# Kernel optimization log

Hardware: AMD Instinct MI355X
Metric: run time of the kernel (lower is better)

The kernel has to match this reference:

```python
import jax, jax.numpy as jnp
import numpy as np

C, S, H = 64, 2048, 512
ITERATIONS = 3

def squash(x, eps=1e-07):
    # per-vector squash along last dim: (|x|^2/(1+|x|^2)) * x/|x|
    sq = jnp.sum(x * x, axis=-1, keepdims=True)
    safe_norm = jnp.sqrt(sq + eps)
    scale = sq / (1.0 + sq)
    return scale * (x / safe_norm)

def setup_inputs() -> dict:
    key = jax.random.key(0)
    k1, k2 = jax.random.split(key)
    x = jax.random.normal(k1, (C * S, H), dtype=jnp.float32)
    # xavier-normal init for Linear(H, H)
    std = np.sqrt(2.0 / (H + H)).astype(np.float32)
    W_weight = jax.random.normal(k2, (H, H), dtype=jnp.float32) * std
    W_bias = jnp.zeros((H,), dtype=jnp.float32)
    return {"x": x, "W_weight": W_weight, "W_bias": W_bias}

def reference(x, W_weight, W_bias):
    xr = x.reshape(C, S, H)
    # e_ij = squash(Linear(x))  -> [C, S, H]
    e_ij = squash(jnp.einsum('csh,oh->cso', xr, W_weight) + W_bias)
    b_ij = jnp.zeros((C, S), dtype=x.dtype)
    c_i = jnp.zeros((C, H), dtype=x.dtype)
    for _ in range(ITERATIONS):
        d_i = jax.nn.softmax(b_ij, axis=1)[..., None]          # [C, S, 1]
        c_i = squash(jnp.sum(d_i * e_ij, axis=1))              # [C, H]
        b_ij = b_ij + jnp.einsum('csh,ch->cs', e_ij, c_i)      # [C, S]
    return c_i
```

## Files before the change

### kernel.cpp

```cpp
#include <hip/hip_runtime.h>
#include <hip/hip_fp16.h>

#define HDIM 512

typedef __fp16 fp16x2 __attribute__((ext_vector_type(2)));
typedef _Float16 h8 __attribute__((ext_vector_type(8)));
typedef __attribute__((ext_vector_type(4))) float floatx4;

__device__ __forceinline__ void lds_barrier() {
  asm volatile("s_waitcnt lgkmcnt(0)\n\ts_barrier" ::: "memory");
}
__device__ __forceinline__ void issue_fence() {
  asm volatile("" ::: "memory");
}

__global__ __launch_bounds__(256) void prep_w_kernel(
    const float* __restrict__ W, _Float16* __restrict__ wf) {
  int i = (blockIdx.x * 256 + threadIdx.x) * 4;
  float4 f = *(const float4*)(W + i);
  wf[i + 0] = (_Float16)f.x;
  wf[i + 1] = (_Float16)f.y;
  wf[i + 2] = (_Float16)f.z;
  wf[i + 3] = (_Float16)f.w;
}

__device__ __forceinline__ void issue_w_dma(const _Float16* wf, _Float16* dst,
                                            int col0, int kt, int widx,
                                            int wn_sub, int wphys) {
#pragma unroll
  for (int q = 0; q < 4; ++q) {
    int i = widx * 4 + q;
    int n_loc = 8 * i + wn_sub;
    int kg_l = wphys ^ (n_loc & 7);
    size_t goff = (size_t)(col0 + n_loc) * HDIM + kt * 64 + kg_l * 8;
    __builtin_amdgcn_global_load_lds(
        (const __attribute__((address_space(1))) void*)(wf + goff),
        (__attribute__((address_space(3))) void*)(dst + i * 512), 16, 0, 0);
  }
}

__global__ __launch_bounds__(256) void gemm_kernel(
    const float* __restrict__ x, const _Float16* __restrict__ wf,
    const float* __restrict__ bias, __half* __restrict__ y,
    float* __restrict__ sq) {
  __shared__ _Float16 xs[128 * 64];
  __shared__ _Float16 wsm[2][128 * 64];

  const int tid = threadIdx.x;
  const int lane = tid & 63;
  const int widx = tid >> 6;
  const int wave_m = widx >> 1, wave_n = widx & 1;
  const int lrow = lane & 15, quad = lane >> 4, l7 = lane & 7;

  const int bid = blockIdx.x;
  const int m_blk = ((bid >> 5) << 3) + (bid & 7);
  const int n_blk = (bid >> 3) & 3;
  const int row0 = m_blk * 128;
  const int col0 = n_blk * 128;
  const int kt0 = bid & 7;

  floatx4 acc[4][4];
#pragma unroll
  for (int i = 0; i < 4; ++i)
#pragma unroll
    for (int j = 0; j < 4; ++j) acc[i][j] = (floatx4){0.f, 0.f, 0.f, 0.f};

  const int xm = tid >> 3;
  const int xkg = tid & 7;
  const int wn_sub = lane >> 3;
  const int wphys = lane & 7;

  const float* xbase = x + (size_t)row0 * HDIM + xkg * 8;
  float4 xr[2][4][2];

  issue_w_dma(wf, &wsm[0][0], col0, kt0, widx, wn_sub, wphys);
  issue_fence();
#pragma unroll
  for (int p = 0; p < 4; ++p) {
    const float* gp = xbase + (size_t)(p * 32 + xm) * HDIM + kt0 * 64;
    xr[0][p][0] = *(const float4*)gp;
    xr[0][p][1] = *(const float4*)(gp + 4);
  }
  issue_fence();
#pragma unroll
  for (int p = 0; p < 4; ++p) {
    const float* gp =
        xbase + (size_t)(p * 32 + xm) * HDIM + ((kt0 + 1) & 7) * 64;
    xr[1][p][0] = *(const float4*)gp;
    xr[1][p][1] = *(const float4*)(gp + 4);
  }

#pragma unroll
  for (int i = 0; i < 8; ++i) {
    lds_barrier();
#pragma unroll
    for (int p = 0; p < 4; ++p) {
      int m = p * 32 + xm;
      union { h8 v8; fp16x2 v2[4]; } u;
      u.v2[0] = __builtin_amdgcn_cvt_pkrtz(xr[i & 1][p][0].x, xr[i & 1][p][0].y);
      u.v2[1] = __builtin_amdgcn_cvt_pkrtz(xr[i & 1][p][0].z, xr[i & 1][p][0].w);
      u.v2[2] = __builtin_amdgcn_cvt_pkrtz(xr[i & 1][p][1].x, xr[i & 1][p][1].y);
      u.v2[3] = __builtin_amdgcn_cvt_pkrtz(xr[i & 1][p][1].z, xr[i & 1][p][1].w);
      int phys = xkg ^ (m & 7);
      *(h8*)&xs[m * 64 + phys * 8] = u.v8;
    }
    lds_barrier();
    if (i < 7)
      issue_w_dma(wf, &wsm[(i + 1) & 1][0], col0, (kt0 + i + 1) & 7, widx,
                  wn_sub, wphys);
    issue_fence();
    if (i < 6) {
      const int ktn = (kt0 + i + 2) & 7;
#pragma unroll
      for (int p = 0; p < 4; ++p) {
        const float* gp = xbase + (size_t)(p * 32 + xm) * HDIM + ktn * 64;
        xr[i & 1][p][0] = *(const float4*)gp;
        xr[i & 1][p][1] = *(const float4*)(gp + 4);
      }
    }
    if (i >= 1 && i <= 5) asm volatile("s_waitcnt vmcnt(20)" ::: "memory");
    if (i == 6) asm volatile("s_waitcnt vmcnt(12)" ::: "memory");
    if (i == 7) asm volatile("s_waitcnt vmcnt(0)" ::: "memory");
    const _Float16* wcur = &wsm[i & 1][0];
#pragma unroll
    for (int ks = 0; ks < 2; ++ks) {
      int physA = (ks * 4 + quad) ^ l7;
      h8 a[4], bh[4];
#pragma unroll
      for (int mt = 0; mt < 4; ++mt) {
        int r = wave_m * 64 + mt * 16 + lrow;
        a[mt] = *(const h8*)&xs[r * 64 + physA * 8];
      }
#pragma unroll
      for (int nt = 0; nt < 4; ++nt) {
        int c = wave_n * 64 + nt * 16 + lrow;
        bh[nt] = *(const h8*)&wcur[c * 64 + physA * 8];
      }
#pragma unroll
      for (int mt = 0; mt < 4; ++mt)
#pragma unroll
        for (int nt = 0; nt < 4; ++nt)
          acc[mt][nt] = __builtin_amdgcn_mfma_f32_16x16x32_f16(
              a[mt], bh[nt], acc[mt][nt], 0, 0, 0);
    }
  }

  int colg[4];
  float bias_v[4];
#pragma unroll
  for (int nt = 0; nt < 4; ++nt) {
    colg[nt] = col0 + wave_n * 64 + nt * 16 + lrow;
    bias_v[nt] = bias[colg[nt]];
  }
#pragma unroll
  for (int mt = 0; mt < 4; ++mt) {
#pragma unroll
    for (int r = 0; r < 4; ++r) {
      int rowg = row0 + wave_m * 64 + mt * 16 + quad * 4 + r;
      float s = 0.f;
#pragma unroll
      for (int nt = 0; nt < 4; ++nt) {
        float yv = acc[mt][nt][r] + bias_v[nt];
        s += yv * yv;
        y[(size_t)rowg * HDIM + colg[nt]] = __float2half(yv);
      }
      s += __shfl_xor(s, 1, 64);
      s += __shfl_xor(s, 2, 64);
      s += __shfl_xor(s, 4, 64);
      s += __shfl_xor(s, 8, 64);
      if (lrow == 0) atomicAdd(&sq[rowg], s);
    }
  }
}

__global__ __launch_bounds__(256) void kbv_kernel(
    const __half* __restrict__ y, const float* __restrict__ sqbuf,
    float* __restrict__ b, const float* __restrict__ c_buf,
    float* __restrict__ u_part, float* __restrict__ den_part) {
  const int w = threadIdx.x >> 6;
  const int lane = threadIdx.x & 63;
  const int wave_g = blockIdx.x * 4 + w;
  const int cap = wave_g >> 6;
  const int chunk = wave_g & 63;
  const int r0 = cap * 2048 + chunk * 32;

  float c8[8];
  {
    const float4* cp = (const float4*)(c_buf + cap * HDIM + lane * 8);
    float4 ca = cp[0], cb = cp[1];
    c8[0] = ca.x; c8[1] = ca.y; c8[2] = ca.z; c8[3] = ca.w;
    c8[4] = cb.x; c8[5] = cb.y; c8[6] = cb.z; c8[7] = cb.w;
  }
  float u8[8] = {0, 0, 0, 0, 0, 0, 0, 0};
  float den = 0.f;

  union U { int4 v; __half hh[8]; };
  U cur[4], nxt[4];
  const __half* yb = y + (size_t)r0 * HDIM + lane * 8;
#pragma unroll
  for (int j = 0; j < 4; ++j) cur[j].v = *(const int4*)(yb + (size_t)j * HDIM);

  for (int g = 0; g < 8; ++g) {
    const int rg = r0 + g * 4;
    if (g < 7) {
#pragma unroll
      for (int j = 0; j < 4; ++j)
        nxt[j].v = *(const int4*)(yb + (size_t)(g * 4 + 4 + j) * HDIM);
    }
    float sc[4], bv[4];
#pragma unroll
    for (int j = 0; j < 4; ++j) {
      float s = sqbuf[rg + j];
      sc[j] = s / ((1.f + s) * sqrtf(s + 1e-7f));
      bv[j] = b[rg + j];
    }
    float dot[4];
#pragma unroll
    for (int j = 0; j < 4; ++j) {
      float d = 0.f;
#pragma unroll
      for (int k = 0; k < 8; ++k) d += __half2float(cur[j].hh[k]) * c8[k];
      dot[j] = d;
    }
#pragma unroll
    for (int s = 1; s < 64; s <<= 1) {
#pragma unroll
      for (int j = 0; j < 4; ++j) dot[j] += __shfl_xor(dot[j], s, 64);
    }
#pragma unroll
    for (int j = 0; j < 4; ++j) {
      float bn = bv[j] + sc[j] * dot[j];
      if (lane == 0) b[rg + j] = bn;
      float wj = __expf(bn);
      den += wj;
      float wsc = wj * sc[j];
#pragma unroll
      for (int k = 0; k < 8; ++k) u8[k] += wsc * __half2float(cur[j].hh[k]);
    }
#pragma unroll
    for (int j = 0; j < 4; ++j) cur[j] = nxt[j];
  }

  __shared__ float lred[4][512];
  __shared__ float ldn[4];
#pragma unroll
  for (int k = 0; k < 8; ++k) lred[w][lane * 8 + k] = u8[k];
  if (lane == 0) ldn[w] = den;
  __syncthreads();
  const int t = threadIdx.x;
  const int blkc = blockIdx.x & 15;
#pragma unroll
  for (int hh = 0; hh < 2; ++hh) {
    int h = hh * 256 + t;
    float v = lred[0][h] + lred[1][h] + lred[2][h] + lred[3][h];
    u_part[((size_t)cap * 16 + blkc) * HDIM + h] = v;
  }
  if (t == 0)
    den_part[cap * 16 + blkc] = ldn[0] + ldn[1] + ldn[2] + ldn[3];
}

__global__ __launch_bounds__(512) void kcsq_kernel(
    const float* __restrict__ u_part, const float* __restrict__ den_part,
    float* __restrict__ out) {
  const int cap = blockIdx.x;
  const int t = threadIdx.x;
  __shared__ float red[512];
  __shared__ float sden;

  if (t < 16) red[t] = den_part[cap * 16 + t];
  __syncthreads();
  if (t == 0) {
    float s = 0.f;
#pragma unroll
    for (int i = 0; i < 16; ++i) s += red[i];
    sden = s;
  }
  __syncthreads();
  const float den = sden;

  float v = 0.f;
  const float* up = u_part + (size_t)cap * 16 * HDIM + t;
#pragma unroll
  for (int ch = 0; ch < 16; ++ch) v += up[ch * HDIM];
  v /= den;

  red[t] = v * v;
  __syncthreads();
  for (int s = 256; s > 0; s >>= 1) {
    if (t < s) red[t] += red[t + s];
    __syncthreads();
  }
  const float sqv = red[0];
  const float scv = sqv / ((1.f + sqv) * sqrtf(sqv + 1e-7f));
  out[cap * HDIM + t] = v * scv;
}

extern "C" void kernel_launch(void* const* d_in, const int* in_sizes, int n_in,
                              void* d_out, int out_size, void* d_ws,
                              size_t ws_size, hipStream_t stream) {
  const float* x = (const float*)d_in[0];
  const float* W = (const float*)d_in[1];
  const float* bias = (const float*)d_in[2];
  float* out = (float*)d_out;
  char* ws = (char*)d_ws;

  __half* y = (__half*)ws;
  float* sq = (float*)(ws + (size_t)134217728);
  float* b = sq + 131072;
  float* c_buf = b + 131072;
  _Float16* wf = (_Float16*)(c_buf + 32768);
  float* u_part = (float*)(wf + 262144);
  float* den_part = u_part + (size_t)64 * 16 * 512;

  (void)hipMemsetAsync(sq, 0,
                       (size_t)(131072 + 131072 + 32768) * sizeof(float),
                       stream);

  prep_w_kernel<<<256, 256, 0, stream>>>(W, wf);
  gemm_kernel<<<4096, 256, 0, stream>>>(x, wf, bias, y, sq);

  for (int it = 0; it < 3; ++it) {
    kbv_kernel<<<1024, 256, 0, stream>>>(y, sq, b, c_buf, u_part, den_part);
    kcsq_kernel<<<64, 512, 0, stream>>>(u_part, den_part,
                                        (it == 2) ? out : c_buf);
  }
}
```

Baseline: 535.4 us.

## Fuse squash and first routing iteration into full-width GEMM epilogue

```diff
diff --git a/kernel.cpp b/kernel.cpp
--- a/kernel.cpp
+++ b/kernel.cpp
@@ -24,159 +24,177 @@
   wf[i + 3] = (_Float16)f.w;
 }
 
-__device__ __forceinline__ void issue_w_dma(const _Float16* wf, _Float16* dst,
-                                            int col0, int kt, int widx,
-                                            int wn_sub, int wphys) {
+#define XS_H (128 * 40)
+#define WS_H (512 * 32)
+
+__device__ __forceinline__ void issue_w_dma(const _Float16* __restrict__ wf,
+                                            _Float16* dst, int kt, int tid,
+                                            int widx) {
 #pragma unroll
   for (int q = 0; q < 4; ++q) {
-    int i = widx * 4 + q;
-    int n_loc = 8 * i + wn_sub;
-    int kg_l = wphys ^ (n_loc & 7);
-    size_t goff = (size_t)(col0 + n_loc) * HDIM + kt * 64 + kg_l * 8;
+    int idx = q * 512 + tid;
+    int n = idx >> 2;
+    int src = (idx & 3) ^ ((n >> 1) & 3);
+    size_t goff = (size_t)n * HDIM + kt * 32 + src * 8;
     __builtin_amdgcn_global_load_lds(
         (const __attribute__((address_space(1))) void*)(wf + goff),
-        (__attribute__((address_space(3))) void*)(dst + i * 512), 16, 0, 0);
-  }
-}
-
-__global__ __launch_bounds__(256) void gemm_kernel(
+        (__attribute__((address_space(3))) void*)(dst +
+                                                  (q * 512 + widx * 64) * 8),
+        16, 0, 0);
+  }
+}
+
+__global__ __launch_bounds__(512, 2) void gemm_kernel(
     const float* __restrict__ x, const _Float16* __restrict__ wf,
-    const float* __restrict__ bias, __half* __restrict__ y,
-    float* __restrict__ sq) {
-  __shared__ _Float16 xs[128 * 64];
-  __shared__ _Float16 wsm[2][128 * 64];
+    const float* __restrict__ bias, __half* __restrict__ e,
+    float* __restrict__ u_part, float* __restrict__ den_part) {
+  __shared__ __align__(16) _Float16 smem[2 * XS_H + 3 * WS_H];
+  _Float16* xs[2] = {smem, smem + XS_H};
+  _Float16* wsm = smem + 2 * XS_H;
 
   const int tid = threadIdx.x;
   const int lane = tid & 63;
   const int widx = tid >> 6;
-  const int wave_m = widx >> 1, wave_n = widx & 1;
-  const int lrow = lane & 15, quad = lane >> 4, l7 = lane & 7;
+  const int wave_m = widx >> 2;
+  const int wave_n = widx & 3;
+  const int lrow = lane & 15, quad = lane >> 4;
 
   const int bid = blockIdx.x;
-  const int m_blk = ((bid >> 5) << 3) + (bid & 7);
-  const int n_blk = (bid >> 3) & 3;
-  const int row0 = m_blk * 128;
-  const int col0 = n_blk * 128;
-  const int kt0 = bid & 7;
-
-  floatx4 acc[4][4];
+  const int row0 = bid * 128;
+
+  const int xrow = tid >> 2;
+  const int xcg = tid & 3;
+  const float* xbase = x + (size_t)(row0 + xrow) * HDIM + xcg * 8;
+
+  floatx4 acc[4][8];
 #pragma unroll
   for (int i = 0; i < 4; ++i)
 #pragma unroll
-    for (int j = 0; j < 4; ++j) acc[i][j] = (floatx4){0.f, 0.f, 0.f, 0.f};
-
-  const int xm = tid >> 3;
-  const int xkg = tid & 7;
-  const int wn_sub = lane >> 3;
-  const int wphys = lane & 7;
-
-  const float* xbase = x + (size_t)row0 * HDIM + xkg * 8;
-  float4 xr[2][4][2];
-
-  issue_w_dma(wf, &wsm[0][0], col0, kt0, widx, wn_sub, wphys);
+    for (int j = 0; j < 8; ++j) acc[i][j] = (floatx4){0.f, 0.f, 0.f, 0.f};
+
+  float4 xr[2][2];
+
+  issue_w_dma(wf, wsm + 0 * WS_H, 0, tid, widx);
   issue_fence();
-#pragma unroll
-  for (int p = 0; p < 4; ++p) {
-    const float* gp = xbase + (size_t)(p * 32 + xm) * HDIM + kt0 * 64;
-    xr[0][p][0] = *(const float4*)gp;
-    xr[0][p][1] = *(const float4*)(gp + 4);
-  }
+  xr[0][0] = *(const float4*)xbase;
+  xr[0][1] = *(const float4*)(xbase + 4);
   issue_fence();
-#pragma unroll
-  for (int p = 0; p < 4; ++p) {
-    const float* gp =
-        xbase + (size_t)(p * 32 + xm) * HDIM + ((kt0 + 1) & 7) * 64;
-    xr[1][p][0] = *(const float4*)gp;
-    xr[1][p][1] = *(const float4*)(gp + 4);
-  }
-
-#pragma unroll
-  for (int i = 0; i < 8; ++i) {
+  issue_w_dma(wf, wsm + 1 * WS_H, 1, tid, widx);
+  issue_fence();
+  xr[1][0] = *(const float4*)(xbase + 32);
+  xr[1][1] = *(const float4*)(xbase + 36);
+  issue_fence();
+
+  const int chunkB = quad ^ ((lrow >> 1) & 3);
+
+#pragma unroll
+  for (int t = 0; t < 16; ++t) {
+    {
+      float4 a0 = xr[t & 1][0], a1 = xr[t & 1][1];
+      union { h8 v8; fp16x2 v2[4]; } u;
+      u.v2[0] = __builtin_amdgcn_cvt_pkrtz(a0.x, a0.y);
+      u.v2[1] = __builtin_amdgcn_cvt_pkrtz(a0.z, a0.w);
+      u.v2[2] = __builtin_amdgcn_cvt_pkrtz(a1.x, a1.y);
+      u.v2[3] = __builtin_amdgcn_cvt_pkrtz(a1.z, a1.w);
+      *(h8*)&xs[t & 1][xrow * 40 + xcg * 8] = u.v8;
+    }
     lds_barrier();
-#pragma unroll
-    for (int p = 0; p < 4; ++p) {
-      int m = p * 32 + xm;
-      union { h8 v8; fp16x2 v2[4]; } u;
-      u.v2[0] = __builtin_amdgcn_cvt_pkrtz(xr[i & 1][p][0].x, xr[i & 1][p][0].y);
-      u.v2[1] = __builtin_amdgcn_cvt_pkrtz(xr[i & 1][p][0].z, xr[i & 1][p][0].w);
-      u.v2[2] = __builtin_amdgcn_cvt_pkrtz(xr[i & 1][p][1].x, xr[i & 1][p][1].y);
-      u.v2[3] = __builtin_amdgcn_cvt_pkrtz(xr[i & 1][p][1].z, xr[i & 1][p][1].w);
-      int phys = xkg ^ (m & 7);
-      *(h8*)&xs[m * 64 + phys * 8] = u.v8;
-    }
-    lds_barrier();
-    if (i < 7)
-      issue_w_dma(wf, &wsm[(i + 1) & 1][0], col0, (kt0 + i + 1) & 7, widx,
-                  wn_sub, wphys);
-    issue_fence();
-    if (i < 6) {
-      const int ktn = (kt0 + i + 2) & 7;
-#pragma unroll
-      for (int p = 0; p < 4; ++p) {
-        const float* gp = xbase + (size_t)(p * 32 + xm) * HDIM + ktn * 64;
-        xr[i & 1][p][0] = *(const float4*)gp;
-        xr[i & 1][p][1] = *(const float4*)(gp + 4);
-      }
-    }
-    if (i >= 1 && i <= 5) asm volatile("s_waitcnt vmcnt(20)" ::: "memory");
-    if (i == 6) asm volatile("s_waitcnt vmcnt(12)" ::: "memory");
-    if (i == 7) asm volatile("s_waitcnt vmcnt(0)" ::: "memory");
-    const _Float16* wcur = &wsm[i & 1][0];
-#pragma unroll
-    for (int ks = 0; ks < 2; ++ks) {
-      int physA = (ks * 4 + quad) ^ l7;
-      h8 a[4], bh[4];
-#pragma unroll
-      for (int mt = 0; mt < 4; ++mt) {
-        int r = wave_m * 64 + mt * 16 + lrow;
-        a[mt] = *(const h8*)&xs[r * 64 + physA * 8];
-      }
-#pragma unroll
-      for (int nt = 0; nt < 4; ++nt) {
-        int c = wave_n * 64 + nt * 16 + lrow;
-        bh[nt] = *(const h8*)&wcur[c * 64 + physA * 8];
-      }
-#pragma unroll
-      for (int mt = 0; mt < 4; ++mt)
-#pragma unroll
-        for (int nt = 0; nt < 4; ++nt)
-          acc[mt][nt] = __builtin_amdgcn_mfma_f32_16x16x32_f16(
-              a[mt], bh[nt], acc[mt][nt], 0, 0, 0);
-    }
-  }
-
-  int colg[4];
-  float bias_v[4];
-#pragma unroll
-  for (int nt = 0; nt < 4; ++nt) {
-    colg[nt] = col0 + wave_n * 64 + nt * 16 + lrow;
+    if (t <= 13) {
+      issue_w_dma(wf, wsm + ((t + 2) % 3) * WS_H, t + 2, tid, widx);
+      issue_fence();
+      const float* gp = xbase + (t + 2) * 32;
+      xr[t & 1][0] = *(const float4*)gp;
+      xr[t & 1][1] = *(const float4*)(gp + 4);
+      issue_fence();
+    }
+    const _Float16* xsr = xs[t & 1];
+    const _Float16* wcur = wsm + (t % 3) * WS_H;
+    h8 a[4], bh[8];
+#pragma unroll
+    for (int mt = 0; mt < 4; ++mt)
+      a[mt] = *(const h8*)&xsr[(wave_m * 64 + mt * 16 + lrow) * 40 + quad * 8];
+#pragma unroll
+    for (int nt = 0; nt < 8; ++nt)
+      bh[nt] =
+          *(const h8*)&wcur[(wave_n * 128 + nt * 16 + lrow) * 32 + chunkB * 8];
+    __builtin_amdgcn_s_setprio(1);
+#pragma unroll
+    for (int mt = 0; mt < 4; ++mt)
+#pragma unroll
+      for (int nt = 0; nt < 8; ++nt)
+        acc[mt][nt] = __builtin_amdgcn_mfma_f32_16x16x32_f16(
+            a[mt], bh[nt], acc[mt][nt], 0, 0, 0);
+    __builtin_amdgcn_s_setprio(0);
+  }
+
+  float* sqp = (float*)smem;
+  float* scs = (float*)smem + 512;
+  float* upl = (float*)smem + 640;
+
+  float bias_v[8];
+  int colg[8];
+#pragma unroll
+  for (int nt = 0; nt < 8; ++nt) {
+    colg[nt] = wave_n * 128 + nt * 16 + lrow;
     bias_v[nt] = bias[colg[nt]];
   }
 #pragma unroll
   for (int mt = 0; mt < 4; ++mt) {
 #pragma unroll
     for (int r = 0; r < 4; ++r) {
-      int rowg = row0 + wave_m * 64 + mt * 16 + quad * 4 + r;
       float s = 0.f;
 #pragma unroll
-      for (int nt = 0; nt < 4; ++nt) {
+      for (int nt = 0; nt < 8; ++nt) {
         float yv = acc[mt][nt][r] + bias_v[nt];
         s += yv * yv;
-        y[(size_t)rowg * HDIM + colg[nt]] = __float2half(yv);
       }
       s += __shfl_xor(s, 1, 64);
       s += __shfl_xor(s, 2, 64);
       s += __shfl_xor(s, 4, 64);
       s += __shfl_xor(s, 8, 64);
-      if (lrow == 0) atomicAdd(&sq[rowg], s);
-    }
-  }
+      if (lrow == 0)
+        sqp[wave_n * 128 + wave_m * 64 + mt * 16 + quad * 4 + r] = s;
+    }
+  }
+  lds_barrier();
+  if (tid < 128) {
+    float s = sqp[tid] + sqp[128 + tid] + sqp[256 + tid] + sqp[384 + tid];
+    scs[tid] = s / ((1.f + s) * sqrtf(s + 1e-7f));
+  }
+  lds_barrier();
+
+  float up[8] = {0.f, 0.f, 0.f, 0.f, 0.f, 0.f, 0.f, 0.f};
+#pragma unroll
+  for (int mt = 0; mt < 4; ++mt) {
+#pragma unroll
+    for (int r = 0; r < 4; ++r) {
+      int row_local = wave_m * 64 + mt * 16 + quad * 4 + r;
+      float scv = scs[row_local];
+      __half* erow = e + (size_t)(row0 + row_local) * HDIM;
+#pragma unroll
+      for (int nt = 0; nt < 8; ++nt) {
+        float ev = (acc[mt][nt][r] + bias_v[nt]) * scv;
+        erow[colg[nt]] = __float2half(ev);
+        up[nt] += ev;
+      }
+    }
+  }
+#pragma unroll
+  for (int nt = 0; nt < 8; ++nt) {
+    float v = up[nt];
+    v += __shfl_xor(v, 16, 64);
+    v += __shfl_xor(v, 32, 64);
+    if (quad == 0) upl[wave_m * 512 + colg[nt]] = v;
+  }
+  lds_barrier();
+  u_part[(size_t)bid * HDIM + tid] = upl[tid] + upl[512 + tid];
+  if (tid == 0) den_part[bid] = 128.0f;
 }
 
 __global__ __launch_bounds__(256) void kbv_kernel(
-    const __half* __restrict__ y, const float* __restrict__ sqbuf,
-    float* __restrict__ b, const float* __restrict__ c_buf,
-    float* __restrict__ u_part, float* __restrict__ den_part) {
+    const __half* __restrict__ e, float* __restrict__ b,
+    const float* __restrict__ c_buf, float* __restrict__ u_part,
+    float* __restrict__ den_part) {
   const int w = threadIdx.x >> 6;
   const int lane = threadIdx.x & 63;
   const int wave_g = blockIdx.x * 4 + w;
@@ -196,7 +214,7 @@
 
   union U { int4 v; __half hh[8]; };
   U cur[4], nxt[4];
-  const __half* yb = y + (size_t)r0 * HDIM + lane * 8;
+  const __half* yb = e + (size_t)r0 * HDIM + lane * 8;
 #pragma unroll
   for (int j = 0; j < 4; ++j) cur[j].v = *(const int4*)(yb + (size_t)j * HDIM);
 
@@ -207,13 +225,9 @@
       for (int j = 0; j < 4; ++j)
         nxt[j].v = *(const int4*)(yb + (size_t)(g * 4 + 4 + j) * HDIM);
     }
-    float sc[4], bv[4];
-#pragma unroll
-    for (int j = 0; j < 4; ++j) {
-      float s = sqbuf[rg + j];
-      sc[j] = s / ((1.f + s) * sqrtf(s + 1e-7f));
-      bv[j] = b[rg + j];
-    }
+    float bv[4];
+#pragma unroll
+    for (int j = 0; j < 4; ++j) bv[j] = b[rg + j];
     float dot[4];
 #pragma unroll
     for (int j = 0; j < 4; ++j) {
@@ -229,13 +243,12 @@
     }
 #pragma unroll
     for (int j = 0; j < 4; ++j) {
-      float bn = bv[j] + sc[j] * dot[j];
+      float bn = bv[j] + dot[j];
       if (lane == 0) b[rg + j] = bn;
       float wj = __expf(bn);
       den += wj;
-      float wsc = wj * sc[j];
-#pragma unroll
-      for (int k = 0; k < 8; ++k) u8[k] += wsc * __half2float(cur[j].hh[k]);
+#pragma unroll
+      for (int k = 0; k < 8; ++k) u8[k] += wj * __half2float(cur[j].hh[k]);
     }
 #pragma unroll
     for (int j = 0; j < 4; ++j) cur[j] = nxt[j];
@@ -304,24 +317,21 @@
   float* out = (float*)d_out;
   char* ws = (char*)d_ws;
 
-  __half* y = (__half*)ws;
-  float* sq = (float*)(ws + (size_t)134217728);
-  float* b = sq + 131072;
+  __half* e = (__half*)ws;
+  float* b = (float*)(ws + (size_t)134217728);
   float* c_buf = b + 131072;
-  _Float16* wf = (_Float16*)(c_buf + 32768);
-  float* u_part = (float*)(wf + 262144);
+  float* u_part = c_buf + 32768;
   float* den_part = u_part + (size_t)64 * 16 * 512;
-
-  (void)hipMemsetAsync(sq, 0,
-                       (size_t)(131072 + 131072 + 32768) * sizeof(float),
-                       stream);
+  _Float16* wf = (_Float16*)(den_part + 1024);
+
+  (void)hipMemsetAsync(b, 0, (size_t)131072 * sizeof(float), stream);
 
   prep_w_kernel<<<256, 256, 0, stream>>>(W, wf);
-  gemm_kernel<<<4096, 256, 0, stream>>>(x, wf, bias, y, sq);
-
-  for (int it = 0; it < 3; ++it) {
-    kbv_kernel<<<1024, 256, 0, stream>>>(y, sq, b, c_buf, u_part, den_part);
-    kcsq_kernel<<<64, 512, 0, stream>>>(u_part, den_part,
-                                        (it == 2) ? out : c_buf);
-  }
-}
+  gemm_kernel<<<1024, 512, 0, stream>>>(x, wf, bias, e, u_part, den_part);
+
+  kcsq_kernel<<<64, 512, 0, stream>>>(u_part, den_part, c_buf);
+  kbv_kernel<<<1024, 256, 0, stream>>>(e, b, c_buf, u_part, den_part);
+  kcsq_kernel<<<64, 512, 0, stream>>>(u_part, den_part, c_buf);
+  kbv_kernel<<<1024, 256, 0, stream>>>(e, b, c_buf, u_part, den_part);
+  kcsq_kernel<<<64, 512, 0, stream>>>(u_part, den_part, out);
+}
```

After: 476.5 us. 11.0% less time.
